# Performance work log

Hardware: AMD Instinct MI355X
Metric: run time of the kernel (lower is better)

The kernel has to match this reference:

```python
import jax, jax.numpy as jnp
import numpy as np
import math

NUM_HEADS = 4


def setup_inputs() -> dict:
    key = jax.random.key(0)
    k1, k2, k3, k4 = jax.random.split(key, 4)
    b, c, f, t = 8, 512, 32, 64
    x = jax.random.normal(k1, (b, c, f, t), dtype=jnp.float32)
    # Conv1d(k=1) weights stored as 2D (out, in); fan-in scaled like torch default
    qkv_w = jax.random.normal(k2, (3 * c, c), dtype=jnp.float32) / math.sqrt(c)
    qkv_b = jax.random.normal(k3, (3 * c,), dtype=jnp.float32) * 0.02
    proj_w = jax.random.normal(k4, (c, c), dtype=jnp.float32) / math.sqrt(c)
    proj_b = jnp.zeros((c,), dtype=jnp.float32)
    return {"x": x, "qkv_w": qkv_w, "qkv_b": qkv_b, "proj_w": proj_w, "proj_b": proj_b}


def reference(x, qkv_w, qkv_b, proj_w, proj_b):
    b, c, f, t = x.shape
    T = f * t
    xr = x.reshape(b, c, T)  # [b, c, T]
    # Note: original forward computes PositionalEncoding2D(x) but discards it.
    qkv = jnp.einsum('oc,bct->bot', qkv_w, xr) + qkv_b[None, :, None]  # [b, 3c, T]
    H = NUM_HEADS
    ch = c // H
    q, k, v = jnp.split(qkv, 3, axis=1)  # each [b, c, T]
    q = q.reshape(b * H, ch, T)
    k = k.reshape(b * H, ch, T)
    v = v.reshape(b * H, ch, T)
    scale = 1.0 / math.sqrt(math.sqrt(ch))
    w = jnp.einsum('bct,bcs->bts', q * scale, k * scale)  # [b*H, T, T]
    w = jax.nn.softmax(w.astype(jnp.float32), axis=-1).astype(q.dtype)
    a = jnp.einsum('bts,bcs->bct', w, v).reshape(b, c, T)
    h = jnp.einsum('oc,bct->bot', proj_w, a) + proj_b[None, :, None]
    return (xr + h).reshape(b, c, f, t)
```

## Files before the change

kernel.cpp:

```cpp
#include <hip/hip_runtime.h>

#define DEV static __device__ __forceinline__

typedef __attribute__((ext_vector_type(8))) short short8;
typedef __attribute__((ext_vector_type(4))) float f32x4;
typedef __attribute__((ext_vector_type(16))) float f32x16;
typedef __attribute__((ext_vector_type(2))) unsigned int uint2v;

DEV unsigned short f2bf(float f) {
    union { float f; unsigned int u; } v; v.f = f;
    unsigned int u = v.u;
    unsigned int r = (u + 0x7fffu + ((u >> 16) & 1u)) >> 16;
    return (unsigned short)r;
}

DEV unsigned int cvtpk(float lo, float hi) {
    unsigned int r;
    asm("v_cvt_pk_bf16_f32 %0, %1, %2" : "=v"(r) : "v"(lo), "v"(hi));
    return r;
}

DEV float vexp2(float x) {
    float r;
    asm("v_exp_f32 %0, %1" : "=v"(r) : "v"(x));
    return r;
}

DEV float pl32_max(float v) {
    union { float f; unsigned u; } c; c.f = v;
    uint2v r = __builtin_amdgcn_permlane32_swap(c.u, c.u, false, false);
    union { unsigned u; float f; } a, b; a.u = r[0]; b.u = r[1];
    return fmaxf(a.f, b.f);
}
DEV float pl32_sum(float v) {
    union { float f; unsigned u; } c; c.f = v;
    uint2v r = __builtin_amdgcn_permlane32_swap(c.u, c.u, false, false);
    union { unsigned u; float f; } a, b; a.u = r[0]; b.u = r[1];
    return a.f + b.f;
}

DEV unsigned short* swp(unsigned short* base, int row, int col, int rs) {
    int a = ((row * rs + col) << 1) ^ ((row & 7) << 4);
    return (unsigned short*)((char*)base + a);
}

DEV void lds_barrier() {
    asm volatile("s_waitcnt lgkmcnt(0)" ::: "memory");
    __builtin_amdgcn_s_barrier();
}

DEV void gload16(const void* g, void* l) {
    __builtin_amdgcn_global_load_lds((const __attribute__((address_space(1))) void*)g,
                                     (__attribute__((address_space(3))) void*)l, 16, 0, 0);
}

__global__ __launch_bounds__(256) void transpose_kernel(const float* __restrict__ x,
                                                        unsigned short* __restrict__ Xt,
                                                        const float* __restrict__ qkv_w,
                                                        const float* __restrict__ proj_w,
                                                        unsigned short* __restrict__ Wq,
                                                        unsigned short* __restrict__ Wp) {
    __shared__ unsigned char lt[64 * 128];
    int b  = blockIdx.z;
    int c0 = blockIdx.y * 64;
    int t0 = blockIdx.x * 64;
    int tid = threadIdx.x;

    {
        int gtid = (((int)blockIdx.z * 8 + (int)blockIdx.y) * 32 + (int)blockIdx.x) * 256 + tid;
        for (int j = gtid; j < 1536 * 512; j += 524288) Wq[j] = f2bf(qkv_w[j]);
        for (int j = gtid; j < 512 * 512;  j += 524288) Wp[j] = f2bf(proj_w[j]);
    }

    int tx = tid & 15, cy0 = tid >> 4;
    for (int p = 0; p < 4; ++p) {
        int cy = cy0 + p * 16;
        const float* src = &x[((size_t)(b * 512 + c0 + cy)) * 2048 + t0 + tx * 4];
        f32x4 v = *(const f32x4*)src;
        unsigned long long pk = (unsigned long long)f2bf(v[0])
                              | ((unsigned long long)f2bf(v[1]) << 16)
                              | ((unsigned long long)f2bf(v[2]) << 32)
                              | ((unsigned long long)f2bf(v[3]) << 48);
        int addr = (cy * 128 + tx * 8) ^ ((cy & 7) << 4);
        *(unsigned long long*)(lt + addr) = pk;
    }
    __syncthreads();
    int c16 = (tid & 3) * 16, tr = tid >> 2;
    unsigned short buf[16];
    for (int i = 0; i < 16; ++i) {
        int c = c16 + i;
        int addr = (c * 128 + tr * 2) ^ ((c & 7) << 4);
        buf[i] = *(unsigned short*)(lt + addr);
    }
    unsigned short* dst = &Xt[((size_t)(b * 2048 + t0 + tr)) * 512 + c0 + c16];
    *(short8*)dst       = *(short8*)&buf[0];
    *(short8*)(dst + 8) = *(short8*)&buf[8];
}

template <int ORIENT>
__global__ __launch_bounds__(256, 2) void gemm_qkv_kernel(
    const unsigned short* __restrict__ Wq,
    const unsigned short* __restrict__ Xt,
    const float* __restrict__ qkv_b,
    unsigned short* __restrict__ Qw,
    unsigned short* __restrict__ Kw,
    unsigned short* __restrict__ Vw) {
    __shared__ unsigned short As[2][128 * 64];
    __shared__ unsigned short Bs[2][128 * 64];
    int b  = blockIdx.z;
    int ot = (ORIENT == 0) ? blockIdx.y : (8 + blockIdx.y);
    int o0 = ot * 128, t0 = blockIdx.x * 128;
    int tid = threadIdx.x, lane = tid & 63, w = tid >> 6;
    int lr = lane >> 4, lc = lane & 15;
    int wr = (w >> 1) * 64, wc = (w & 1) * 64;
    f32x4 acc[4][4];
    for (int m = 0; m < 4; m++)
        for (int n = 0; n < 4; n++) acc[m][n] = (f32x4){0.f, 0.f, 0.f, 0.f};

    int r8 = lane >> 3, ck = lane & 7;
    int sc8 = (ck ^ r8) * 8;

    const unsigned short* Wbase = &Wq[(size_t)o0 * 512];
    const unsigned short* Xbase = &Xt[((size_t)(b * 2048) + t0) * 512];

    #define QKV_STAGE(buf, ks)                                                        \
        _Pragma("unroll")                                                             \
        for (int p = 0; p < 4; p++) {                                                 \
            int rowblk = (w * 4 + p) * 8;                                             \
            gload16(&Wbase[(size_t)(rowblk + r8) * 512 + (ks) * 64 + sc8],            \
                    &As[buf][rowblk * 64]);                                           \
            gload16(&Xbase[(size_t)(rowblk + r8) * 512 + (ks) * 64 + sc8],            \
                    &Bs[buf][rowblk * 64]);                                           \
        }

    QKV_STAGE(0, 0);
    asm volatile("s_waitcnt vmcnt(0)" ::: "memory");
    __builtin_amdgcn_s_barrier();
    for (int t = 0; t < 8; ++t) {
        int cur = t & 1;
        if (t < 7) { QKV_STAGE(cur ^ 1, t + 1); }
        unsigned short* Ab = (unsigned short*)As[cur];
        unsigned short* Bb = (unsigned short*)Bs[cur];
        #pragma unroll
        for (int kk = 0; kk < 64; kk += 32) {
            int kb = kk + lr * 8;
            short8 af[4], bfv[4];
            if (ORIENT == 0) {
                for (int m = 0; m < 4; m++) af[m]  = *(const short8*)swp(Bb, wr + m * 16 + lc, kb, 64);
                for (int n = 0; n < 4; n++) bfv[n] = *(const short8*)swp(Ab, wc + n * 16 + lc, kb, 64);
            } else {
                for (int m = 0; m < 4; m++) af[m]  = *(const short8*)swp(Ab, wr + m * 16 + lc, kb, 64);
                for (int n = 0; n < 4; n++) bfv[n] = *(const short8*)swp(Bb, wc + n * 16 + lc, kb, 64);
            }
            for (int m = 0; m < 4; m++)
                for (int n = 0; n < 4; n++)
                    acc[m][n] = __builtin_amdgcn_mfma_f32_16x16x32_bf16(af[m], bfv[n], acc[m][n], 0, 0, 0);
        }
        asm volatile("s_waitcnt vmcnt(0)" ::: "memory");
        __builtin_amdgcn_s_barrier();
    }
    const float scale_k = 0.29730177875068026f;
    const float scale_q = 0.42891498953885586f;
    for (int m = 0; m < 4; m++)
        for (int n = 0; n < 4; n++)
            for (int r = 0; r < 4; r++) {
                int row = wr + m * 16 + lr * 4 + r;
                int col = wc + n * 16 + lc;
                float val = acc[m][n][r];
                if (ORIENT == 0) {
                    int t = t0 + row;
                    int o = o0 + col;
                    float sc = (o < 512) ? scale_q : scale_k;
                    val = (val + qkv_b[o]) * sc;
                    if (o < 512) {
                        int h = o >> 7, cc = o & 127;
                        Qw[((size_t)((b * 4 + h) * 2048 + t)) * 128 + cc] = f2bf(val);
                    } else {
                        int oo = o - 512;
                        int h = oo >> 7, cc = oo & 127;
                        Kw[((size_t)((b * 4 + h) * 2048 + t)) * 128 + cc] = f2bf(val);
                    }
                } else {
                    int o = o0 + row;
                    int t = t0 + col;
                    val += qkv_b[o];
                    int oo = o - 1024;
                    int h = oo >> 7, cc = oo & 127;
                    Vw[((size_t)((b * 4 + h) * 128 + cc)) * 2048 + t] = f2bf(val);
                }
            }
}

__global__ __launch_bounds__(256, 2) void attn_kernel(
    const unsigned short* __restrict__ Qw,
    const unsigned short* __restrict__ Kw,
    const unsigned short* __restrict__ Vw,
    unsigned short* __restrict__ Aw) {
    __shared__ unsigned short lds[32768];
    int bid = blockIdx.x;
    int bh = bid & 31;
    int t0 = (bid >> 5) * 128;
    int tid = threadIdx.x, lane = tid & 63, w = tid >> 6;
    int l31 = lane & 31, hi = lane >> 5;
    int qrow = w * 32;

    const unsigned short* Kbase = &Kw[(size_t)bh * 2048 * 128];
    const unsigned short* Vbase = &Vw[(size_t)bh * 128 * 2048];

    short8 qf[8];
    #pragma unroll
    for (int st = 0; st < 8; st++)
        qf[st] = *(const short8*)&Qw[((size_t)bh * 2048 + t0 + qrow + l31) * 128 + st * 16 + hi * 8];

    f32x16 oacc[4];
    #pragma unroll
    for (int ct = 0; ct < 4; ct++)
        #pragma unroll
        for (int i = 0; i < 16; i++) oacc[ct][i] = 0.f;
    float mst = -1e30f, lst = 0.f;

    int kr = tid >> 4, ko = (tid & 15) * 8;
    int vr = tid >> 3, vo = (tid & 7) * 8;

    short8 kreg[4], vreg[4];
    #pragma unroll
    for (int p = 0; p < 4; p++)
        kreg[p] = *(const short8*)&Kbase[(size_t)(kr + p * 16) * 128 + ko];
    #pragma unroll
    for (int p = 0; p < 4; p++)
        vreg[p] = *(const short8*)&Vbase[(size_t)(vr + p * 32) * 2048 + vo];

    for (int it = 0; it < 32; ++it) {
        int cur = it & 1;
        unsigned short* Kb = lds + cur * 8192;
        unsigned short* Vb = lds + 16384 + cur * 8192;
        #pragma unroll
        for (int p = 0; p < 4; p++) *(short8*)swp(Kb, kr + p * 16, ko, 128) = kreg[p];
        #pragma unroll
        for (int p = 0; p < 4; p++) *(short8*)swp(Vb, vr + p * 32, vo, 64) = vreg[p];
        if (it + 1 < 32) {
            int s1 = (it + 1) * 64;
            #pragma unroll
            for (int p = 0; p < 4; p++)
                kreg[p] = *(const short8*)&Kbase[(size_t)(s1 + kr + p * 16) * 128 + ko];
            #pragma unroll
            for (int p = 0; p < 4; p++)
                vreg[p] = *(const short8*)&Vbase[(size_t)(vr + p * 32) * 2048 + s1 + vo];
        }
        lds_barrier();

        f32x16 s0, s1v;
        #pragma unroll
        for (int i = 0; i < 16; i++) { s0[i] = 0.f; s1v[i] = 0.f; }
        __builtin_amdgcn_s_setprio(1);
        #pragma unroll
        for (int st = 0; st < 8; st++) {
            short8 k0 = *(const short8*)swp(Kb, l31,      st * 16 + hi * 8, 128);
            short8 k1 = *(const short8*)swp(Kb, 32 + l31, st * 16 + hi * 8, 128);
            s0  = __builtin_amdgcn_mfma_f32_32x32x16_bf16(k0, qf[st], s0, 0, 0, 0);
            s1v = __builtin_amdgcn_mfma_f32_32x32x16_bf16(k1, qf[st], s1v, 0, 0, 0);
        }
        __builtin_amdgcn_s_setprio(0);

        float m16[16];
        #pragma unroll
        for (int i = 0; i < 16; i++) m16[i] = fmaxf(s0[i], s1v[i]);
        #pragma unroll
        for (int sdt = 8; sdt > 0; sdt >>= 1)
            #pragma unroll
            for (int i = 0; i < 8; i++)
                if (i < sdt) m16[i] = fmaxf(m16[i], m16[i + sdt]);
        float mx = pl32_max(m16[0]);
        if (!__all(mx <= mst + 11.541560327111707f)) {
            float mnew = fmaxf(mst, mx);
            float resc = vexp2(mst - mnew);
            mst = mnew;
            lst *= resc;
            #pragma unroll
            for (int ct = 0; ct < 4; ct++)
                #pragma unroll
                for (int i = 0; i < 16; i++) oacc[ct][i] *= resc;
        }
        float pe[32];
        #pragma unroll
        for (int i = 0; i < 16; i++) pe[i]      = vexp2(s0[i]  - mst);
        #pragma unroll
        for (int i = 0; i < 16; i++) pe[16 + i] = vexp2(s1v[i] - mst);
        float a16[16];
        #pragma unroll
        for (int i = 0; i < 16; i++) a16[i] = pe[i] + pe[16 + i];
        #pragma unroll
        for (int sdt = 8; sdt > 0; sdt >>= 1)
            #pragma unroll
            for (int i = 0; i < 8; i++)
                if (i < sdt) a16[i] = a16[i] + a16[i + sdt];
        lst += pl32_sum(a16[0]);

        short8 pf[4];
        #pragma unroll
        for (int st = 0; st < 4; st++) {
            unsigned X0 = cvtpk(pe[st * 8 + 0], pe[st * 8 + 1]);
            unsigned X1 = cvtpk(pe[st * 8 + 2], pe[st * 8 + 3]);
            unsigned Y0 = cvtpk(pe[st * 8 + 4], pe[st * 8 + 5]);
            unsigned Y1 = cvtpk(pe[st * 8 + 6], pe[st * 8 + 7]);
            uint2v r0 = __builtin_amdgcn_permlane32_swap(X0, Y0, false, false);
            uint2v r1 = __builtin_amdgcn_permlane32_swap(X1, Y1, false, false);
            union { unsigned u[4]; short8 s; } uu;
            uu.u[0] = r0[0];
            uu.u[1] = r1[0];
            uu.u[2] = r0[1];
            uu.u[3] = r1[1];
            pf[st] = uu.s;
        }

        __builtin_amdgcn_s_setprio(1);
        #pragma unroll
        for (int ct = 0; ct < 4; ct++)
            #pragma unroll
            for (int st = 0; st < 4; st++) {
                short8 va = *(const short8*)swp(Vb, ct * 32 + l31, st * 16 + hi * 8, 64);
                oacc[ct] = __builtin_amdgcn_mfma_f32_32x32x16_bf16(va, pf[st], oacc[ct], 0, 0, 0);
            }
        __builtin_amdgcn_s_setprio(0);
    }

    __syncthreads();
    unsigned short* ep = lds + w * 4096;
    float invl = 1.f / lst;
    #pragma unroll
    for (int ct = 0; ct < 4; ct++)
        #pragma unroll
        for (int i = 0; i < 8; i++) {
            int c = (2 * i & 3) + 8 * (i >> 1) + 4 * hi + 32 * ct;
            unsigned d = cvtpk(oacc[ct][2 * i] * invl, oacc[ct][2 * i + 1] * invl);
            *(unsigned*)swp(ep, l31, c, 128) = d;
        }
    asm volatile("" ::: "memory");
    int q = lane >> 1, hf = lane & 1;
    int b = bh >> 2, h = bh & 3;
    #pragma unroll
    for (int p = 0; p < 8; p++) {
        short8 v = *(const short8*)swp(ep, q, hf * 64 + p * 8, 128);
        *(short8*)&Aw[((size_t)(b * 2048) + t0 + qrow + q) * 512 + h * 128 + hf * 64 + p * 8] = v;
    }
}

#define LP 72
__global__ __launch_bounds__(256, 2) void gemm_proj_kernel(
    const unsigned short* __restrict__ Wp,
    const unsigned short* __restrict__ Aw,
    const float* __restrict__ proj_b,
    const float* __restrict__ x,
    float* __restrict__ out) {
    __shared__ unsigned short Ws[2][128][LP];
    __shared__ unsigned short Bs[2][128][LP];
    int b  = blockIdx.z;
    int o0 = blockIdx.y * 128, t0 = blockIdx.x * 128;
    int tid = threadIdx.x, lane = tid & 63, w = tid >> 6;
    int lr = lane >> 4, lc = lane & 15;
    int wr = (w >> 1) * 64, wc = (w & 1) * 64;
    f32x4 acc[4][4];
    for (int m = 0; m < 4; m++)
        for (int n = 0; n < 4; n++) acc[m][n] = (f32x4){0.f, 0.f, 0.f, 0.f};
    int srow = tid >> 3, soff = (tid & 7) * 8;

    short8 wreg[4], breg[4];
    #pragma unroll
    for (int p = 0; p < 4; p++) {
        wreg[p] = *(const short8*)&Wp[(size_t)(o0 + srow + p * 32) * 512 + soff];
        breg[p] = *(const short8*)&Aw[((size_t)(b * 2048) + t0 + srow + p * 32) * 512 + soff];
    }
    for (int t = 0; t < 8; ++t) {
        int cur = t & 1;
        #pragma unroll
        for (int p = 0; p < 4; p++) {
            *(short8*)&Ws[cur][srow + p * 32][soff] = wreg[p];
            *(short8*)&Bs[cur][srow + p * 32][soff] = breg[p];
        }
        if (t < 7) {
            int k1 = (t + 1) * 64;
            #pragma unroll
            for (int p = 0; p < 4; p++) {
                wreg[p] = *(const short8*)&Wp[(size_t)(o0 + srow + p * 32) * 512 + k1 + soff];
                breg[p] = *(const short8*)&Aw[((size_t)(b * 2048) + t0 + srow + p * 32) * 512 + k1 + soff];
            }
        }
        lds_barrier();
        for (int kk = 0; kk < 64; kk += 32) {
            int kb = kk + lr * 8;
            short8 af[4], bfv[4];
            for (int m = 0; m < 4; m++) af[m]  = *(const short8*)&Ws[cur][wr + m * 16 + lc][kb];
            for (int n = 0; n < 4; n++) bfv[n] = *(const short8*)&Bs[cur][wc + n * 16 + lc][kb];
            for (int m = 0; m < 4; m++)
                for (int n = 0; n < 4; n++)
                    acc[m][n] = __builtin_amdgcn_mfma_f32_16x16x32_bf16(af[m], bfv[n], acc[m][n], 0, 0, 0);
        }
        __builtin_amdgcn_s_barrier();
    }
    for (int m = 0; m < 4; m++)
        for (int n = 0; n < 4; n++)
            for (int r = 0; r < 4; r++) {
                int o = o0 + wr + m * 16 + lr * 4 + r;
                int t = t0 + wc + n * 16 + lc;
                size_t idx = ((size_t)(b * 512) + o) * 2048 + t;
                out[idx] = x[idx] + acc[m][n][r] + proj_b[o];
            }
}

extern "C" void kernel_launch(void* const* d_in, const int* in_sizes, int n_in,
                              void* d_out, int out_size, void* d_ws, size_t ws_size,
                              hipStream_t stream) {
    const float* x      = (const float*)d_in[0];
    const float* qkv_w  = (const float*)d_in[1];
    const float* qkv_b  = (const float*)d_in[2];
    const float* proj_w = (const float*)d_in[3];
    const float* proj_b = (const float*)d_in[4];
    float* out = (float*)d_out;

    unsigned short* ws = (unsigned short*)d_ws;
    unsigned short* Wq = ws;
    unsigned short* Wp = Wq + (size_t)1536 * 512;
    unsigned short* Xt = Wp + (size_t)512 * 512;
    unsigned short* Qw = Xt + (size_t)8 * 2048 * 512;
    unsigned short* Kw = Qw + (size_t)32 * 2048 * 128;
    unsigned short* Vw = Kw + (size_t)32 * 2048 * 128;
    unsigned short* Aw = Vw + (size_t)32 * 2048 * 128;

    transpose_kernel<<<dim3(32, 8, 8), dim3(256), 0, stream>>>(x, Xt, qkv_w, proj_w, Wq, Wp);
    gemm_qkv_kernel<0><<<dim3(16, 8, 8), dim3(256), 0, stream>>>(Wq, Xt, qkv_b, Qw, Kw, Vw);
    gemm_qkv_kernel<1><<<dim3(16, 4, 8), dim3(256), 0, stream>>>(Wq, Xt, qkv_b, Qw, Kw, Vw);
    attn_kernel<<<dim3(512), dim3(256), 0, stream>>>(Qw, Kw, Vw, Aw);
    gemm_proj_kernel<<<dim3(16, 4, 8), dim3(256), 0, stream>>>(Wp, Aw, proj_b, x, out);
}
```

Before: 161.0 us.

## Split attention keys in two halves with a separate combine kernel

Attention now splits the key sequence into two halves, so the grid doubles to 1024 blocks, each handling 32-key tiles and using half the LDS so more blocks can be resident per CU. Each half writes a partial bf16 output plus its running max and sum, and a new combine kernel merges the halves with log-sum-exp weights into the head-interleaved layout. The aim is more parallelism and occupancy on the MI355X's many CUs. The cost is an extra launch, an extra round trip of the partial outputs through global memory, smaller MFMA work per barrier, and one more bf16 rounding step.

```diff
diff --git a/kernel.cpp b/kernel.cpp
--- a/kernel.cpp
+++ b/kernel.cpp
@@ -13,6 +13,10 @@
     unsigned int r = (u + 0x7fffu + ((u >> 16) & 1u)) >> 16;
     return (unsigned short)r;
 }
+DEV float bf2f(unsigned short s) {
+    union { unsigned int u; float f; } v; v.u = ((unsigned int)s) << 16;
+    return v.f;
+}
 
 DEV unsigned int cvtpk(float lo, float hi) {
     unsigned int r;
@@ -52,6 +56,22 @@
 DEV void gload16(const void* g, void* l) {
     __builtin_amdgcn_global_load_lds((const __attribute__((address_space(1))) void*)g,
                                      (__attribute__((address_space(3))) void*)l, 16, 0, 0);
+}
+
+DEV short8 mk_pf(float v0, float v1, float v2, float v3,
+                 float v4, float v5, float v6, float v7) {
+    unsigned X0 = cvtpk(v0, v1);
+    unsigned X1 = cvtpk(v2, v3);
+    unsigned Y0 = cvtpk(v4, v5);
+    unsigned Y1 = cvtpk(v6, v7);
+    uint2v r0 = __builtin_amdgcn_permlane32_swap(X0, Y0, false, false);
+    uint2v r1 = __builtin_amdgcn_permlane32_swap(X1, Y1, false, false);
+    union { unsigned u[4]; short8 s; } uu;
+    uu.u[0] = r0[0];
+    uu.u[1] = r1[0];
+    uu.u[2] = r0[1];
+    uu.u[3] = r1[1];
+    return uu.s;
 }
 
 __global__ __launch_bounds__(256) void transpose_kernel(const float* __restrict__ x,
@@ -191,15 +211,19 @@
             }
 }
 
-__global__ __launch_bounds__(256, 2) void attn_kernel(
+__global__ __launch_bounds__(256, 4) void attn_kernel(
     const unsigned short* __restrict__ Qw,
     const unsigned short* __restrict__ Kw,
     const unsigned short* __restrict__ Vw,
-    unsigned short* __restrict__ Aw) {
-    __shared__ unsigned short lds[32768];
+    unsigned short* __restrict__ Op,
+    float* __restrict__ Ml) {
+    __shared__ unsigned short lds[16384];
     int bid = blockIdx.x;
     int bh = bid & 31;
-    int t0 = (bid >> 5) * 128;
+    int rest = bid >> 5;
+    int t0 = (rest & 15) * 128;
+    int side = rest >> 4;
+    int sbase = side * 1024;
     int tid = threadIdx.x, lane = tid & 63, w = tid >> 6;
     int l31 = lane & 31, hi = lane >> 5;
     int qrow = w * 32;
@@ -220,57 +244,55 @@
     float mst = -1e30f, lst = 0.f;
 
     int kr = tid >> 4, ko = (tid & 15) * 8;
-    int vr = tid >> 3, vo = (tid & 7) * 8;
-
-    short8 kreg[4], vreg[4];
-    #pragma unroll
-    for (int p = 0; p < 4; p++)
-        kreg[p] = *(const short8*)&Kbase[(size_t)(kr + p * 16) * 128 + ko];
-    #pragma unroll
-    for (int p = 0; p < 4; p++)
-        vreg[p] = *(const short8*)&Vbase[(size_t)(vr + p * 32) * 2048 + vo];
+    int vr = tid >> 2, vo = (tid & 3) * 8;
+
+    short8 kreg[2], vreg[2];
+    #pragma unroll
+    for (int p = 0; p < 2; p++)
+        kreg[p] = *(const short8*)&Kbase[(size_t)(sbase + kr + p * 16) * 128 + ko];
+    #pragma unroll
+    for (int p = 0; p < 2; p++)
+        vreg[p] = *(const short8*)&Vbase[(size_t)(vr + p * 64) * 2048 + sbase + vo];
 
     for (int it = 0; it < 32; ++it) {
         int cur = it & 1;
-        unsigned short* Kb = lds + cur * 8192;
-        unsigned short* Vb = lds + 16384 + cur * 8192;
-        #pragma unroll
-        for (int p = 0; p < 4; p++) *(short8*)swp(Kb, kr + p * 16, ko, 128) = kreg[p];
-        #pragma unroll
-        for (int p = 0; p < 4; p++) *(short8*)swp(Vb, vr + p * 32, vo, 64) = vreg[p];
+        unsigned short* Kb = lds + cur * 4096;
+        unsigned short* Vb = lds + 8192 + cur * 4096;
+        #pragma unroll
+        for (int p = 0; p < 2; p++) *(short8*)swp(Kb, kr + p * 16, ko, 128) = kreg[p];
+        #pragma unroll
+        for (int p = 0; p < 2; p++) *(short8*)swp(Vb, vr + p * 64, vo, 32) = vreg[p];
         if (it + 1 < 32) {
-            int s1 = (it + 1) * 64;
-            #pragma unroll
-            for (int p = 0; p < 4; p++)
+            int s1 = sbase + (it + 1) * 32;
+            #pragma unroll
+            for (int p = 0; p < 2; p++)
                 kreg[p] = *(const short8*)&Kbase[(size_t)(s1 + kr + p * 16) * 128 + ko];
             #pragma unroll
-            for (int p = 0; p < 4; p++)
-                vreg[p] = *(const short8*)&Vbase[(size_t)(vr + p * 32) * 2048 + s1 + vo];
+            for (int p = 0; p < 2; p++)
+                vreg[p] = *(const short8*)&Vbase[(size_t)(vr + p * 64) * 2048 + s1 + vo];
         }
         lds_barrier();
 
-        f32x16 s0, s1v;
-        #pragma unroll
-        for (int i = 0; i < 16; i++) { s0[i] = 0.f; s1v[i] = 0.f; }
+        f32x16 s0;
+        #pragma unroll
+        for (int i = 0; i < 16; i++) s0[i] = 0.f;
         __builtin_amdgcn_s_setprio(1);
         #pragma unroll
         for (int st = 0; st < 8; st++) {
-            short8 k0 = *(const short8*)swp(Kb, l31,      st * 16 + hi * 8, 128);
-            short8 k1 = *(const short8*)swp(Kb, 32 + l31, st * 16 + hi * 8, 128);
-            s0  = __builtin_amdgcn_mfma_f32_32x32x16_bf16(k0, qf[st], s0, 0, 0, 0);
-            s1v = __builtin_amdgcn_mfma_f32_32x32x16_bf16(k1, qf[st], s1v, 0, 0, 0);
+            short8 k0 = *(const short8*)swp(Kb, l31, st * 16 + hi * 8, 128);
+            s0 = __builtin_amdgcn_mfma_f32_32x32x16_bf16(k0, qf[st], s0, 0, 0, 0);
         }
         __builtin_amdgcn_s_setprio(0);
 
-        float m16[16];
-        #pragma unroll
-        for (int i = 0; i < 16; i++) m16[i] = fmaxf(s0[i], s1v[i]);
-        #pragma unroll
-        for (int sdt = 8; sdt > 0; sdt >>= 1)
-            #pragma unroll
-            for (int i = 0; i < 8; i++)
-                if (i < sdt) m16[i] = fmaxf(m16[i], m16[i + sdt]);
-        float mx = pl32_max(m16[0]);
+        float m8[8];
+        #pragma unroll
+        for (int i = 0; i < 8; i++) m8[i] = fmaxf(s0[i], s0[i + 8]);
+        #pragma unroll
+        for (int sdt = 4; sdt > 0; sdt >>= 1)
+            #pragma unroll
+            for (int i = 0; i < 4; i++)
+                if (i < sdt) m8[i] = fmaxf(m8[i], m8[i + sdt]);
+        float mx = pl32_max(m8[0]);
         if (!__all(mx <= mst + 11.541560327111707f)) {
             float mnew = fmaxf(mst, mx);
             float resc = vexp2(mst - mnew);
@@ -281,44 +303,29 @@
                 #pragma unroll
                 for (int i = 0; i < 16; i++) oacc[ct][i] *= resc;
         }
-        float pe[32];
-        #pragma unroll
-        for (int i = 0; i < 16; i++) pe[i]      = vexp2(s0[i]  - mst);
-        #pragma unroll
-        for (int i = 0; i < 16; i++) pe[16 + i] = vexp2(s1v[i] - mst);
-        float a16[16];
-        #pragma unroll
-        for (int i = 0; i < 16; i++) a16[i] = pe[i] + pe[16 + i];
-        #pragma unroll
-        for (int sdt = 8; sdt > 0; sdt >>= 1)
-            #pragma unroll
-            for (int i = 0; i < 8; i++)
-                if (i < sdt) a16[i] = a16[i] + a16[i + sdt];
-        lst += pl32_sum(a16[0]);
-
-        short8 pf[4];
-        #pragma unroll
-        for (int st = 0; st < 4; st++) {
-            unsigned X0 = cvtpk(pe[st * 8 + 0], pe[st * 8 + 1]);
-            unsigned X1 = cvtpk(pe[st * 8 + 2], pe[st * 8 + 3]);
-            unsigned Y0 = cvtpk(pe[st * 8 + 4], pe[st * 8 + 5]);
-            unsigned Y1 = cvtpk(pe[st * 8 + 6], pe[st * 8 + 7]);
-            uint2v r0 = __builtin_amdgcn_permlane32_swap(X0, Y0, false, false);
-            uint2v r1 = __builtin_amdgcn_permlane32_swap(X1, Y1, false, false);
-            union { unsigned u[4]; short8 s; } uu;
-            uu.u[0] = r0[0];
-            uu.u[1] = r1[0];
-            uu.u[2] = r0[1];
-            uu.u[3] = r1[1];
-            pf[st] = uu.s;
-        }
+        float pe[16];
+        #pragma unroll
+        for (int i = 0; i < 16; i++) pe[i] = vexp2(s0[i] - mst);
+        float a8[8];
+        #pragma unroll
+        for (int i = 0; i < 8; i++) a8[i] = pe[i] + pe[i + 8];
+        #pragma unroll
+        for (int sdt = 4; sdt > 0; sdt >>= 1)
+            #pragma unroll
+            for (int i = 0; i < 4; i++)
+                if (i < sdt) a8[i] = a8[i] + a8[i + sdt];
+        lst += pl32_sum(a8[0]);
+
+        short8 pf[2];
+        pf[0] = mk_pf(pe[0], pe[1], pe[2], pe[3], pe[4], pe[5], pe[6], pe[7]);
+        pf[1] = mk_pf(pe[8], pe[9], pe[10], pe[11], pe[12], pe[13], pe[14], pe[15]);
 
         __builtin_amdgcn_s_setprio(1);
         #pragma unroll
         for (int ct = 0; ct < 4; ct++)
             #pragma unroll
-            for (int st = 0; st < 4; st++) {
-                short8 va = *(const short8*)swp(Vb, ct * 32 + l31, st * 16 + hi * 8, 64);
+            for (int st = 0; st < 2; st++) {
+                short8 va = *(const short8*)swp(Vb, ct * 32 + l31, st * 16 + hi * 8, 32);
                 oacc[ct] = __builtin_amdgcn_mfma_f32_32x32x16_bf16(va, pf[st], oacc[ct], 0, 0, 0);
             }
         __builtin_amdgcn_s_setprio(0);
@@ -337,12 +344,45 @@
         }
     asm volatile("" ::: "memory");
     int q = lane >> 1, hf = lane & 1;
-    int b = bh >> 2, h = bh & 3;
+    unsigned short* Opb = Op + ((size_t)(side * 32 + bh) * 2048 + t0 + qrow) * 128;
+    float* Mlb = Ml + ((size_t)(side * 32 + bh) * 2048) * 2;
     #pragma unroll
     for (int p = 0; p < 8; p++) {
         short8 v = *(const short8*)swp(ep, q, hf * 64 + p * 8, 128);
-        *(short8*)&Aw[((size_t)(b * 2048) + t0 + qrow + q) * 512 + h * 128 + hf * 64 + p * 8] = v;
-    }
+        *(short8*)&Opb[(size_t)q * 128 + hf * 64 + p * 8] = v;
+    }
+    if (hi == 0) {
+        Mlb[(size_t)(t0 + qrow + l31) * 2 + 0] = mst;
+        Mlb[(size_t)(t0 + qrow + l31) * 2 + 1] = lst;
+    }
+}
+
+__global__ __launch_bounds__(256) void combine_kernel(
+    const unsigned short* __restrict__ Op,
+    const float* __restrict__ Ml,
+    unsigned short* __restrict__ Aw) {
+    int g = blockIdx.x * 256 + threadIdx.x;
+    int c8 = g & 15;
+    int row = g >> 4;
+    int bh = row >> 11;
+    int t  = row & 2047;
+    const size_t SIDE = (size_t)32 * 2048 * 128;
+    size_t o0 = (size_t)row * 128 + c8 * 8;
+    float m0 = Ml[(size_t)row * 2], l0 = Ml[(size_t)row * 2 + 1];
+    float m1 = Ml[((size_t)32 * 2048 + row) * 2], l1 = Ml[((size_t)32 * 2048 + row) * 2 + 1];
+    float M = fmaxf(m0, m1);
+    float w0 = vexp2(m0 - M) * l0;
+    float w1 = vexp2(m1 - M) * l1;
+    float inv = 1.f / (w0 + w1);
+    w0 *= inv; w1 *= inv;
+    short8 a = *(const short8*)&Op[o0];
+    short8 b = *(const short8*)&Op[SIDE + o0];
+    unsigned short outv[8];
+    #pragma unroll
+    for (int j = 0; j < 8; j++)
+        outv[j] = f2bf(bf2f((unsigned short)a[j]) * w0 + bf2f((unsigned short)b[j]) * w1);
+    int bq = bh >> 2, h = bh & 3;
+    *(short8*)&Aw[((size_t)(bq * 2048) + t) * 512 + h * 128 + c8 * 8] = *(short8*)outv;
 }
 
 #define LP 72
@@ -425,10 +465,13 @@
     unsigned short* Kw = Qw + (size_t)32 * 2048 * 128;
     unsigned short* Vw = Kw + (size_t)32 * 2048 * 128;
     unsigned short* Aw = Vw + (size_t)32 * 2048 * 128;
+    unsigned short* Opp = Aw + (size_t)8 * 2048 * 512;
+    float* Ml = (float*)(Opp + (size_t)2 * 32 * 2048 * 128);
 
     transpose_kernel<<<dim3(32, 8, 8), dim3(256), 0, stream>>>(x, Xt, qkv_w, proj_w, Wq, Wp);
     gemm_qkv_kernel<0><<<dim3(16, 8, 8), dim3(256), 0, stream>>>(Wq, Xt, qkv_b, Qw, Kw, Vw);
     gemm_qkv_kernel<1><<<dim3(16, 4, 8), dim3(256), 0, stream>>>(Wq, Xt, qkv_b, Qw, Kw, Vw);
-    attn_kernel<<<dim3(512), dim3(256), 0, stream>>>(Qw, Kw, Vw, Aw);
+    attn_kernel<<<dim3(1024), dim3(256), 0, stream>>>(Qw, Kw, Vw, Opp, Ml);
+    combine_kernel<<<dim3(4096), dim3(256), 0, stream>>>(Opp, Ml, Aw);
     gemm_proj_kernel<<<dim3(16, 4, 8), dim3(256), 0, stream>>>(Wp, Aw, proj_b, x, out);
 }
```

Result: slower. 315.8 us (+96.2%).
